# Optimization experiments

Measured on AMD Instinct MI355X. Metric: run time of the kernel, lower is better.

Reference implementation:

```python
import jax, jax.numpy as jnp
import numpy as np

N_EMBD = 1024
N_HEADS = 16
B, T = 4, 2048
EPS = 1e-5


def setup_inputs() -> dict:
    key = jax.random.key(0)
    ks = jax.random.split(key, 8)
    C = N_EMBD
    s = 0.02
    return {
        "x": jax.random.normal(ks[0], (B, T, C), dtype=jnp.float32),
        "ln1_w": jnp.ones((C,), jnp.float32),
        "ln1_b": jnp.zeros((C,), jnp.float32),
        "qkv_w": jax.random.normal(ks[1], (C, 3 * C), jnp.float32) * s,
        "qkv_b": jnp.zeros((3 * C,), jnp.float32),
        "proj_w": jax.random.normal(ks[2], (C, C), jnp.float32) * s,
        "proj_b": jnp.zeros((C,), jnp.float32),
        "ln2_w": jnp.ones((C,), jnp.float32),
        "ln2_b": jnp.zeros((C,), jnp.float32),
        "ff_w1": jax.random.normal(ks[3], (C, 4 * C), jnp.float32) * s,
        "ff_b1": jnp.zeros((4 * C,), jnp.float32),
        "ff_w2": jax.random.normal(ks[4], (4 * C, C), jnp.float32) * s,
        "ff_b2": jnp.zeros((C,), jnp.float32),
    }


def _layernorm(x, w, b):
    mu = jnp.mean(x, axis=-1, keepdims=True)
    var = jnp.mean(jnp.square(x - mu), axis=-1, keepdims=True)
    return (x - mu) * jax.lax.rsqrt(var + EPS) * w + b


def _block(x, ln1_w, ln1_b, qkv_w, qkv_b, proj_w, proj_b,
           ln2_w, ln2_b, ff_w1, ff_b1, ff_w2, ff_b2):
    Bb, Tt, C = x.shape
    hd = C // N_HEADS
    h = _layernorm(x, ln1_w, ln1_b)
    qkv = h @ qkv_w + qkv_b  # [B,T,3C]
    q, k, v = jnp.split(qkv, 3, axis=-1)
    q = q.reshape(Bb, Tt, N_HEADS, hd)
    k = k.reshape(Bb, Tt, N_HEADS, hd)
    v = v.reshape(Bb, Tt, N_HEADS, hd)
    # NOTE: original scales by 1/sqrt(C) (full embed dim), not 1/sqrt(head_dim)
    att = jnp.einsum("bqhd,bkhd->bhqk", q, k) * (1.0 / C ** 0.5)
    causal = jnp.tril(jnp.ones((Tt, Tt), dtype=bool))
    att = jnp.where(causal[None, None], att, -jnp.inf)
    att = jax.nn.softmax(att, axis=-1)
    y = jnp.einsum("bhqk,bkhd->bqhd", att, v).reshape(Bb, Tt, C)
    x = x + y @ proj_w + proj_b
    h2 = _layernorm(x, ln2_w, ln2_b)
    ff = jax.nn.relu(h2 @ ff_w1 + ff_b1) @ ff_w2 + ff_b2
    return x + ff


def reference(x, ln1_w, ln1_b, qkv_w, qkv_b, proj_w, proj_b,
              ln2_w, ln2_b, ff_w1, ff_b1, ff_w2, ff_b2):
    return _block(x, ln1_w, ln1_b, qkv_w, qkv_b, proj_w, proj_b,
                  ln2_w, ln2_b, ff_w1, ff_b1, ff_w2, ff_b2)
```

## Files before the change

### kernel.cpp

```cpp
#include <hip/hip_runtime.h>


typedef __attribute__((ext_vector_type(8))) short shortx8;
typedef __attribute__((ext_vector_type(4))) float floatx4;

__device__ __forceinline__ short f2bf(float f) {
  unsigned u = __builtin_bit_cast(unsigned, f);
  u = (u + 0x7fffu + ((u >> 16) & 1u)) >> 16;
  return (short)u;
}

__global__ __launch_bounds__(256)
void transpose_cast(const float* __restrict__ in, short* __restrict__ out,
                    int K, int N) {
  __shared__ float tile[32][33];
  const int n0 = blockIdx.x * 32, k0 = blockIdx.y * 32;
  const int tx = threadIdx.x & 31, ty = threadIdx.x >> 5;
  for (int i = 0; i < 32; i += 8)
    tile[ty + i][tx] = in[(size_t)(k0 + ty + i) * N + n0 + tx];
  __syncthreads();
  for (int i = 0; i < 32; i += 8)
    out[(size_t)(n0 + ty + i) * K + k0 + tx] = f2bf(tile[tx][ty + i]);
}

__global__ __launch_bounds__(256)
void layernorm_kernel(const float* __restrict__ x, const float* __restrict__ w,
                      const float* __restrict__ bta, short* __restrict__ out) {
  const int C = 1024;
  const int row = blockIdx.x;
  const float4 v = ((const float4*)(x + (size_t)row * C))[threadIdx.x];
  float s1 = v.x + v.y + v.z + v.w;
  float s2 = v.x * v.x + v.y * v.y + v.z * v.z + v.w * v.w;
  for (int m = 1; m < 64; m <<= 1) { s1 += __shfl_xor(s1, m); s2 += __shfl_xor(s2, m); }
  __shared__ float r1[4], r2[4];
  const int wid = threadIdx.x >> 6, lane = threadIdx.x & 63;
  if (lane == 0) { r1[wid] = s1; r2[wid] = s2; }
  __syncthreads();
  s1 = r1[0] + r1[1] + r1[2] + r1[3];
  s2 = r2[0] + r2[1] + r2[2] + r2[3];
  const float mean = s1 * (1.0f / C);
  const float var = s2 * (1.0f / C) - mean * mean;
  const float rs = rsqrtf(var + 1e-5f);
  const float4 wv = ((const float4*)w)[threadIdx.x];
  const float4 bv = ((const float4*)bta)[threadIdx.x];
  short4 o;
  o.x = f2bf((v.x - mean) * rs * wv.x + bv.x);
  o.y = f2bf((v.y - mean) * rs * wv.y + bv.y);
  o.z = f2bf((v.z - mean) * rs * wv.z + bv.z);
  o.w = f2bf((v.w - mean) * rs * wv.w + bv.w);
  *(short4*)(out + (size_t)row * C + threadIdx.x * 4) = o;
}

template<int FLAGS, typename OutT>
__global__ __launch_bounds__(256, 4)
void gemm_bt(const short* __restrict__ A, int lda,
             const short* __restrict__ Bt, int ldb,
             const float* __restrict__ bias, const float* __restrict__ resid,
             OutT* __restrict__ C, int M, int N, int K) {
  constexpr bool RELU = (FLAGS & 1) != 0;
  constexpr bool RESID = (FLAGS & 2) != 0;
  __shared__ short As[2][128 * 32];
  __shared__ short Bs[2][128 * 32];
  int bmi, bni;
  {
    const int nb = gridDim.x, mb = gridDim.y;
    const int g = blockIdx.x + nb * blockIdx.y;
    if ((mb & 7) == 0) {
      const int xcd = g & 7, l = g >> 3;
      bmi = xcd * (mb >> 3) + l / nb;
      bni = l % nb;
    } else { bmi = blockIdx.y; bni = blockIdx.x; }
  }
  const int bm0 = bmi * 128, bn0 = bni * 128;
  const int tid = threadIdx.x, wid = tid >> 6, lane = tid & 63;
  const int quad = lane >> 4, l15 = lane & 15;
  const int wm = wid & 1, wn = wid >> 1;
  const int srow = lane >> 2, scol = (lane & 3) * 8;
  floatx4 acc[4][4] = {};
  for (int k0 = 0; k0 < K; k0 += 64) {
    for (int i = 0; i < 2; ++i) {
      const int r0 = (wid * 2 + i) * 16;
      const short* ga = A + (size_t)(bm0 + r0 + srow) * lda + k0 + scol;
      const short* gb = Bt + (size_t)(bn0 + r0 + srow) * ldb + k0 + scol;
      __builtin_amdgcn_global_load_lds(
          (const __attribute__((address_space(1))) void*)ga,
          (__attribute__((address_space(3))) void*)&As[0][r0 * 32], 16, 0, 0);
      __builtin_amdgcn_global_load_lds(
          (const __attribute__((address_space(1))) void*)(ga + 32),
          (__attribute__((address_space(3))) void*)&As[1][r0 * 32], 16, 0, 0);
      __builtin_amdgcn_global_load_lds(
          (const __attribute__((address_space(1))) void*)gb,
          (__attribute__((address_space(3))) void*)&Bs[0][r0 * 32], 16, 0, 0);
      __builtin_amdgcn_global_load_lds(
          (const __attribute__((address_space(1))) void*)(gb + 32),
          (__attribute__((address_space(3))) void*)&Bs[1][r0 * 32], 16, 0, 0);
    }
    asm volatile("s_waitcnt vmcnt(0)" ::: "memory");
    __syncthreads();
    {
      shortx8 af[4], bfr[4];
#pragma unroll
      for (int i = 0; i < 4; ++i)
        af[i] = *(const shortx8*)&As[0][(wm * 64 + i * 16 + l15) * 32 + quad * 8];
#pragma unroll
      for (int j = 0; j < 4; ++j)
        bfr[j] = *(const shortx8*)&Bs[0][(wn * 64 + j * 16 + l15) * 32 + quad * 8];
#pragma unroll
      for (int i = 0; i < 4; ++i)
#pragma unroll
        for (int j = 0; j < 4; ++j)
          acc[i][j] = __builtin_amdgcn_mfma_f32_16x16x32_bf16(af[i], bfr[j], acc[i][j], 0, 0, 0);
    }
    {
      shortx8 af[4], bfr[4];
#pragma unroll
      for (int i = 0; i < 4; ++i)
        af[i] = *(const shortx8*)&As[1][(wm * 64 + i * 16 + l15) * 32 + quad * 8];
#pragma unroll
      for (int j = 0; j < 4; ++j)
        bfr[j] = *(const shortx8*)&Bs[1][(wn * 64 + j * 16 + l15) * 32 + quad * 8];
#pragma unroll
      for (int i = 0; i < 4; ++i)
#pragma unroll
        for (int j = 0; j < 4; ++j)
          acc[i][j] = __builtin_amdgcn_mfma_f32_16x16x32_bf16(af[i], bfr[j], acc[i][j], 0, 0, 0);
    }
    __syncthreads();
  }
#pragma unroll
  for (int i = 0; i < 4; ++i) {
    const int row = bm0 + wm * 64 + i * 16 + quad * 4;
#pragma unroll
    for (int j = 0; j < 4; ++j) {
      const int col = bn0 + wn * 64 + j * 16 + l15;
      const float bb = bias[col];
#pragma unroll
      for (int r = 0; r < 4; ++r) {
        float v = acc[i][j][r] + bb;
        if (RELU) v = fmaxf(v, 0.0f);
        if (RESID) v += resid[(size_t)(row + r) * N + col];
        if constexpr (sizeof(OutT) == 2)
          C[(size_t)(row + r) * N + col] = f2bf(v);
        else
          C[(size_t)(row + r) * N + col] = v;
      }
    }
  }
}

#define ATTN_SLOTS 80
#define ATTN_SLOT_F 4160

__global__ __launch_bounds__(256)
void attention_chunk(const short* __restrict__ qkv, short* __restrict__ y,
                     float* __restrict__ part) {
  constexpr int T = 2048, C = 1024, HD = 64, S3 = 3072;
  __shared__ short Ks[64 * 72];
  __shared__ short Vt[64 * 72];
  __shared__ short Ps[4][16 * 72];
  const int x = blockIdx.x, h = blockIdx.y, b = blockIdx.z;
  int qb, ch;
  if (x < 8)       { qb = x;                 ch = 0; }
  else if (x < 24) { qb = 8 + ((x - 8) >> 1);  ch = (x - 8) & 1; }
  else if (x < 48) { qb = 16 + (x - 24) / 3;   ch = (x - 24) % 3; }
  else             { qb = 24 + ((x - 48) >> 2); ch = (x - 48) & 3; }
  const int kt0 = ch * 8;
  const int kt1 = min(kt0 + 8, qb + 1);
  const int tid = threadIdx.x, wid = tid >> 6, lane = tid & 63;
  const int quad = lane >> 4, l15 = lane & 15;
  const size_t base = (size_t)b * T * S3;
  const int q0 = qb * 64 + wid * 16;
  const short* Qp = qkv + base + (size_t)(q0 + l15) * S3 + h * HD;
  const shortx8 qf0 = *(const shortx8*)(Qp + quad * 8);
  const shortx8 qf1 = *(const shortx8*)(Qp + 32 + quad * 8);
  floatx4 o[4] = {};
  float lsum[4] = {0.f, 0.f, 0.f, 0.f};
  const float scale2 = 0.03125f * 1.44269504088896f;
  const int skey = tid >> 2, sd = (tid & 3) * 16;
  const int vkp = tid & 31, vdb = tid >> 5;
  const int vkE = (vkp >> 4) * 32 + (vkp & 15);
  const short* Kbase = qkv + base + C + h * HD;
  const short* Vbase = qkv + base + 2 * C + h * HD;
  shortx8 pk0, pk1, pv0, pv1;
  {
    const short* Kp = Kbase + (size_t)(kt0 * 64 + skey) * S3 + sd;
    pk0 = *(const shortx8*)Kp;
    pk1 = *(const shortx8*)(Kp + 8);
    const short* Vp = Vbase + (size_t)(kt0 * 64 + vkE) * S3 + vdb * 8;
    pv0 = *(const shortx8*)Vp;
    pv1 = *(const shortx8*)(Vp + 16 * S3);
  }
  for (int kt = kt0; kt < kt1; ++kt) {
    const int key0 = kt * 64;
    __syncthreads();
    *(shortx8*)&Ks[skey * 72 + sd] = pk0;
    *(shortx8*)&Ks[skey * 72 + sd + 8] = pk1;
#pragma unroll
    for (int j = 0; j < 8; ++j) {
      short2 pr = make_short2(pv0[j], pv1[j]);
      *(short2*)&Vt[(vdb * 8 + j) * 72 + 2 * vkp] = pr;
    }
    __syncthreads();
    if (kt + 1 < kt1) {
      const int kn = key0 + 64;
      const short* Kp = Kbase + (size_t)(kn + skey) * S3 + sd;
      pk0 = *(const shortx8*)Kp;
      pk1 = *(const shortx8*)(Kp + 8);
      const short* Vp = Vbase + (size_t)(kn + vkE) * S3 + vdb * 8;
      pv0 = *(const shortx8*)Vp;
      pv1 = *(const shortx8*)(Vp + 16 * S3);
    }
    floatx4 s[4];
#pragma unroll
    for (int nt = 0; nt < 4; ++nt) {
      const short* kb = &Ks[(nt * 16 + l15) * 72 + quad * 8];
      floatx4 a = {};
      a = __builtin_amdgcn_mfma_f32_16x16x32_bf16(qf0, *(const shortx8*)kb, a, 0, 0, 0);
      a = __builtin_amdgcn_mfma_f32_16x16x32_bf16(qf1, *(const shortx8*)(kb + 32), a, 0, 0, 0);
      s[nt] = a;
    }
    short* pw = &Ps[wid][0];
    const bool diag = (kt == qb);
#pragma unroll
    for (int r = 0; r < 4; ++r) {
      float pr[4];
#pragma unroll
      for (int nt = 0; nt < 4; ++nt) {
        float sv = s[nt][r] * scale2;
        if (diag) {
          const int key = key0 + nt * 16 + l15;
          const int q = q0 + quad * 4 + r;
          if (key > q) sv = -INFINITY;
        }
        const float p = exp2f(sv);
        lsum[r] += p;
        pr[nt] = p;
      }
      unsigned w0, w1;
      asm("v_cvt_pk_bf16_f32 %0, %1, %2" : "=v"(w0) : "v"(pr[0]), "v"(pr[1]));
      asm("v_cvt_pk_bf16_f32 %0, %1, %2" : "=v"(w1) : "v"(pr[2]), "v"(pr[3]));
      unsigned* prow = (unsigned*)&pw[(quad * 4 + r) * 72];
      prow[l15] = w0;
      prow[16 + l15] = w1;
    }
    asm volatile("s_waitcnt lgkmcnt(0)" ::: "memory");
#pragma unroll
    for (int kf = 0; kf < 2; ++kf) {
      const shortx8 pa = *(const shortx8*)&Ps[wid][l15 * 72 + kf * 32 + quad * 8];
#pragma unroll
      for (int dt = 0; dt < 4; ++dt) {
        const shortx8 vb = *(const shortx8*)&Vt[(dt * 16 + l15) * 72 + kf * 32 + quad * 8];
        o[dt] = __builtin_amdgcn_mfma_f32_16x16x32_bf16(pa, vb, o[dt], 0, 0, 0);
      }
    }
  }
  float ls[4];
#pragma unroll
  for (int r = 0; r < 4; ++r) {
    float s = lsum[r];
    for (int off = 1; off < 16; off <<= 1) s += __shfl_xor(s, off);
    ls[r] = s;
  }
  if (x < 8) {
#pragma unroll
    for (int dt = 0; dt < 4; ++dt)
#pragma unroll
      for (int r = 0; r < 4; ++r) {
        const int q = q0 + quad * 4 + r;
        y[((size_t)b * T + q) * C + h * HD + dt * 16 + l15] =
            f2bf(o[dt][r] / ls[r]);
      }
  } else {
    float* pp = part + ((size_t)(b * 16 + h) * ATTN_SLOTS + x) * ATTN_SLOT_F;
    const int qw = wid * 16;
#pragma unroll
    for (int dt = 0; dt < 4; ++dt)
#pragma unroll
      for (int r = 0; r < 4; ++r)
        pp[(qw + quad * 4 + r) * 64 + dt * 16 + l15] = o[dt][r];
    if (l15 == 0)
#pragma unroll
      for (int r = 0; r < 4; ++r)
        pp[4096 + qw + quad * 4 + r] = ls[r];
  }
}

__global__ __launch_bounds__(256)
void attn_reduce(const float* __restrict__ part, short* __restrict__ y) {
  constexpr int T = 2048, C = 1024;
  const int qb = 8 + blockIdx.x, h = blockIdx.y, b = blockIdx.z;
  const int c = qb / 8 + 1;
  int slot0;
  if (qb < 16)      slot0 = 8 + 2 * (qb - 8);
  else if (qb < 24) slot0 = 24 + 3 * (qb - 16);
  else              slot0 = 48 + 4 * (qb - 24);
  const float* rb = part + ((size_t)(b * 16 + h) * ATTN_SLOTS + slot0) * ATTN_SLOT_F;
  const int t = threadIdx.x;
  const int q = t >> 2, dg = (t & 3) * 16;
  float acc[16] = {};
  float ls = 0.f;
  for (int ci = 0; ci < c; ++ci) {
    const float* pp = rb + (size_t)ci * ATTN_SLOT_F;
    const float4* op = (const float4*)(pp + q * 64 + dg);
#pragma unroll
    for (int i = 0; i < 4; ++i) {
      float4 v = op[i];
      acc[4 * i + 0] += v.x; acc[4 * i + 1] += v.y;
      acc[4 * i + 2] += v.z; acc[4 * i + 3] += v.w;
    }
    ls += pp[4096 + q];
  }
  const float inv = 1.0f / ls;
  short o16[16];
#pragma unroll
  for (int i = 0; i < 16; ++i) o16[i] = f2bf(acc[i] * inv);
  short* yp = y + ((size_t)b * T + qb * 64 + q) * C + h * 64 + dg;
  *(shortx8*)yp = *(shortx8*)&o16[0];
  *(shortx8*)(yp + 8) = *(shortx8*)&o16[8];
}

__global__ __launch_bounds__(256)
void attention_kernel(const short* __restrict__ qkv, short* __restrict__ y) {
  constexpr int T = 2048, C = 1024, HD = 64, S3 = 3072;
  __shared__ short Ks[64 * 72];
  __shared__ short Vt[64 * 72];
  __shared__ short Ps[4][16 * 72];
  const int qb = blockIdx.x, h = blockIdx.y, b = blockIdx.z;
  const int tid = threadIdx.x, wid = tid >> 6, lane = tid & 63;
  const int quad = lane >> 4, l15 = lane & 15;
  const size_t base = (size_t)b * T * S3;
  const int q0 = qb * 64 + wid * 16;
  const short* Qp = qkv + base + (size_t)(q0 + l15) * S3 + h * HD;
  const shortx8 qf0 = *(const shortx8*)(Qp + quad * 8);
  const shortx8 qf1 = *(const shortx8*)(Qp + 32 + quad * 8);
  floatx4 o[4] = {};
  float lsum[4] = {0.f, 0.f, 0.f, 0.f};
  const float scale2 = 0.03125f * 1.44269504088896f;
  const int skey = tid >> 2, sd = (tid & 3) * 16;
  const int vkp = tid & 31, vdb = tid >> 5;
  for (int kt = 0; kt <= qb; ++kt) {
    const int key0 = kt * 64;
    __syncthreads();
    {
      const short* Kp = qkv + base + (size_t)(key0 + skey) * S3 + C + h * HD + sd;
      shortx8 ka = *(const shortx8*)Kp;
      shortx8 kb = *(const shortx8*)(Kp + 8);
      *(shortx8*)&Ks[skey * 72 + sd] = ka;
      *(shortx8*)&Ks[skey * 72 + sd + 8] = kb;
      const short* Vp = qkv + base + (size_t)(key0 + 2 * vkp) * S3 + 2 * C + h * HD + vdb * 8;
      shortx8 va = *(const shortx8*)Vp;
      shortx8 vb = *(const shortx8*)(Vp + S3);
#pragma unroll
      for (int j = 0; j < 8; ++j) {
        short2 pr = make_short2(va[j], vb[j]);
        *(short2*)&Vt[(vdb * 8 + j) * 72 + 2 * vkp] = pr;
      }
    }
    __syncthreads();
    floatx4 s[4];
#pragma unroll
    for (int nt = 0; nt < 4; ++nt) {
      const short* kb = &Ks[(nt * 16 + l15) * 72 + quad * 8];
      floatx4 a = {};
      a = __builtin_amdgcn_mfma_f32_16x16x32_bf16(qf0, *(const shortx8*)kb, a, 0, 0, 0);
      a = __builtin_amdgcn_mfma_f32_16x16x32_bf16(qf1, *(const shortx8*)(kb + 32), a, 0, 0, 0);
      s[nt] = a;
    }
    short* pw = &Ps[wid][0];
    const bool diag = (kt == qb);
#pragma unroll
    for (int nt = 0; nt < 4; ++nt)
#pragma unroll
      for (int r = 0; r < 4; ++r) {
        float sv = s[nt][r] * scale2;
        if (diag) {
          const int key = key0 + nt * 16 + l15;
          const int q = q0 + quad * 4 + r;
          if (key > q) sv = -INFINITY;
        }
        const float p = exp2f(sv);
        lsum[r] += p;
        pw[(quad * 4 + r) * 72 + nt * 16 + l15] = f2bf(p);
      }
    asm volatile("s_waitcnt lgkmcnt(0)" ::: "memory");
#pragma unroll
    for (int kf = 0; kf < 2; ++kf) {
      const shortx8 pa = *(const shortx8*)&Ps[wid][l15 * 72 + kf * 32 + quad * 8];
#pragma unroll
      for (int dt = 0; dt < 4; ++dt) {
        const shortx8 vb = *(const shortx8*)&Vt[(dt * 16 + l15) * 72 + kf * 32 + quad * 8];
        o[dt] = __builtin_amdgcn_mfma_f32_16x16x32_bf16(pa, vb, o[dt], 0, 0, 0);
      }
    }
  }
  float inv[4];
#pragma unroll
  for (int r = 0; r < 4; ++r) {
    float s = lsum[r];
    for (int off = 1; off < 16; off <<= 1) s += __shfl_xor(s, off);
    inv[r] = 1.0f / s;
  }
#pragma unroll
  for (int dt = 0; dt < 4; ++dt)
#pragma unroll
    for (int r = 0; r < 4; ++r) {
      const int q = q0 + quad * 4 + r;
      y[((size_t)b * T + q) * C + h * HD + dt * 16 + l15] = f2bf(o[dt][r] * inv[r]);
    }
}

extern "C" void kernel_launch(void* const* d_in, const int* in_sizes, int n_in,
                              void* d_out, int out_size, void* d_ws, size_t ws_size,
                              hipStream_t stream) {
  const float* x      = (const float*)d_in[0];
  const float* ln1_w  = (const float*)d_in[1];
  const float* ln1_b  = (const float*)d_in[2];
  const float* qkv_w  = (const float*)d_in[3];
  const float* qkv_b  = (const float*)d_in[4];
  const float* proj_w = (const float*)d_in[5];
  const float* proj_b = (const float*)d_in[6];
  const float* ln2_w  = (const float*)d_in[7];
  const float* ln2_b  = (const float*)d_in[8];
  const float* ff_w1  = (const float*)d_in[9];
  const float* ff_b1  = (const float*)d_in[10];
  const float* ff_w2  = (const float*)d_in[11];
  const float* ff_b2  = (const float*)d_in[12];
  float* out = (float*)d_out;

  char* p = (char*)d_ws;
  short* wT_qkv  = (short*)p; p += (size_t)3072 * 1024 * 2;
  short* wT_proj = (short*)p; p += (size_t)1024 * 1024 * 2;
  short* wT_ff1  = (short*)p; p += (size_t)4096 * 1024 * 2;
  short* wT_ff2  = (short*)p; p += (size_t)1024 * 4096 * 2;
  short* act16   = (short*)p; p += (size_t)8192 * 1024 * 2;
  short* big     = (short*)p; p += (size_t)8192 * 4096 * 2;
  float* part    = (float*)p;
  const size_t need = (size_t)(p - (char*)d_ws) +
                      (size_t)64 * ATTN_SLOTS * ATTN_SLOT_F * 4;
  const bool split = (ws_size >= need);

  transpose_cast<<<dim3(96, 32), 256, 0, stream>>>(qkv_w, wT_qkv, 1024, 3072);
  transpose_cast<<<dim3(32, 32), 256, 0, stream>>>(proj_w, wT_proj, 1024, 1024);
  transpose_cast<<<dim3(128, 32), 256, 0, stream>>>(ff_w1, wT_ff1, 1024, 4096);
  transpose_cast<<<dim3(32, 128), 256, 0, stream>>>(ff_w2, wT_ff2, 4096, 1024);

  layernorm_kernel<<<8192, 256, 0, stream>>>(x, ln1_w, ln1_b, act16);
  gemm_bt<0, short><<<dim3(24, 64), 256, 0, stream>>>(
      act16, 1024, wT_qkv, 1024, qkv_b, nullptr, big, 8192, 3072, 1024);
  if (split) {
    attention_chunk<<<dim3(ATTN_SLOTS, 16, 4), 256, 0, stream>>>(big, act16, part);
    attn_reduce<<<dim3(24, 16, 4), 256, 0, stream>>>(part, act16);
  } else {
    attention_kernel<<<dim3(32, 16, 4), 256, 0, stream>>>(big, act16);
  }
  gemm_bt<2, float><<<dim3(8, 64), 256, 0, stream>>>(
      act16, 1024, wT_proj, 1024, proj_b, x, out, 8192, 1024, 1024);
  layernorm_kernel<<<8192, 256, 0, stream>>>(out, ln2_w, ln2_b, act16);
  gemm_bt<1, short><<<dim3(32, 64), 256, 0, stream>>>(
      act16, 1024, wT_ff1, 1024, ff_b1, nullptr, big, 8192, 4096, 1024);
  gemm_bt<2, float><<<dim3(8, 64), 256, 0, stream>>>(
      big, 4096, wT_ff2, 4096, ff_b2, out, out, 8192, 1024, 4096);
}
```

Measured before the change: 498.1 us.

## Process two query blocks per attention chunk to reuse staged K/V tiles

Each attention_chunk workgroup now covers 128 queries (two 64-row sub-blocks) instead of 64, so every K/V tile loaded into shared memory feeds twice the MFMA work. The grid shrinks from 80 to 40 slots per head, the partial-slot size doubles, and attn_reduce is rewritten to combine 128-row slots with 32 columns per thread. This is meant to halve global K/V traffic and staging overhead. In exchange it doubles the accumulator registers, with launch bounds set to allow 4 blocks, and reduces the number of workgroups, which may lower occupancy and worsen load balance.

```diff
diff --git a/kernel.cpp b/kernel.cpp
--- a/kernel.cpp
+++ b/kernel.cpp
@@ -148,10 +148,10 @@
   }
 }
 
-#define ATTN_SLOTS 80
-#define ATTN_SLOT_F 4160
-
-__global__ __launch_bounds__(256)
+#define ATTN_SLOTS 40
+#define ATTN_SLOT_F 8320
+
+__global__ __launch_bounds__(256, 4)
 void attention_chunk(const short* __restrict__ qkv, short* __restrict__ y,
                      float* __restrict__ part) {
   constexpr int T = 2048, C = 1024, HD = 64, S3 = 3072;
@@ -159,22 +159,26 @@
   __shared__ short Vt[64 * 72];
   __shared__ short Ps[4][16 * 72];
   const int x = blockIdx.x, h = blockIdx.y, b = blockIdx.z;
-  int qb, ch;
-  if (x < 8)       { qb = x;                 ch = 0; }
-  else if (x < 24) { qb = 8 + ((x - 8) >> 1);  ch = (x - 8) & 1; }
-  else if (x < 48) { qb = 16 + (x - 24) / 3;   ch = (x - 24) % 3; }
-  else             { qb = 24 + ((x - 48) >> 2); ch = (x - 48) & 3; }
+  int qb0, ch;
+  if (x < 4)       { qb0 = x;                    ch = 0; }
+  else if (x < 12) { qb0 = 4 + ((x - 4) >> 1);   ch = (x - 4) & 1; }
+  else if (x < 24) { qb0 = 8 + (x - 12) / 3;     ch = (x - 12) % 3; }
+  else             { qb0 = 12 + ((x - 24) >> 2); ch = (x - 24) & 3; }
   const int kt0 = ch * 8;
-  const int kt1 = min(kt0 + 8, qb + 1);
+  const int kt1 = min(kt0 + 8, 2 * qb0 + 2);
   const int tid = threadIdx.x, wid = tid >> 6, lane = tid & 63;
   const int quad = lane >> 4, l15 = lane & 15;
   const size_t base = (size_t)b * T * S3;
-  const int q0 = qb * 64 + wid * 16;
-  const short* Qp = qkv + base + (size_t)(q0 + l15) * S3 + h * HD;
-  const shortx8 qf0 = *(const shortx8*)(Qp + quad * 8);
-  const shortx8 qf1 = *(const shortx8*)(Qp + 32 + quad * 8);
-  floatx4 o[4] = {};
-  float lsum[4] = {0.f, 0.f, 0.f, 0.f};
+  const int Q0 = qb0 * 128;
+  shortx8 qf[2][2];
+#pragma unroll
+  for (int s = 0; s < 2; ++s) {
+    const short* Qp = qkv + base + (size_t)(Q0 + s * 64 + wid * 16 + l15) * S3 + h * HD;
+    qf[s][0] = *(const shortx8*)(Qp + quad * 8);
+    qf[s][1] = *(const shortx8*)(Qp + 32 + quad * 8);
+  }
+  floatx4 o[2][4] = {};
+  float lsum[2][4] = {};
   const float scale2 = 0.03125f * 1.44269504088896f;
   const int skey = tid >> 2, sd = (tid & 3) * 16;
   const int vkp = tid & 31, vdb = tid >> 5;
@@ -210,113 +214,127 @@
       pv0 = *(const shortx8*)Vp;
       pv1 = *(const shortx8*)(Vp + 16 * S3);
     }
-    floatx4 s[4];
-#pragma unroll
-    for (int nt = 0; nt < 4; ++nt) {
-      const short* kb = &Ks[(nt * 16 + l15) * 72 + quad * 8];
-      floatx4 a = {};
-      a = __builtin_amdgcn_mfma_f32_16x16x32_bf16(qf0, *(const shortx8*)kb, a, 0, 0, 0);
-      a = __builtin_amdgcn_mfma_f32_16x16x32_bf16(qf1, *(const shortx8*)(kb + 32), a, 0, 0, 0);
-      s[nt] = a;
-    }
-    short* pw = &Ps[wid][0];
-    const bool diag = (kt == qb);
+#pragma unroll
+    for (int s = 0; s < 2; ++s) {
+      const int lim = 2 * qb0 + s;
+      if (kt > lim) continue;
+      const int q0s = Q0 + s * 64 + wid * 16;
+      floatx4 sc[4];
+#pragma unroll
+      for (int nt = 0; nt < 4; ++nt) {
+        const short* kb = &Ks[(nt * 16 + l15) * 72 + quad * 8];
+        floatx4 a = {};
+        a = __builtin_amdgcn_mfma_f32_16x16x32_bf16(qf[s][0], *(const shortx8*)kb, a, 0, 0, 0);
+        a = __builtin_amdgcn_mfma_f32_16x16x32_bf16(qf[s][1], *(const shortx8*)(kb + 32), a, 0, 0, 0);
+        sc[nt] = a;
+      }
+      short* pw = &Ps[wid][0];
+      const bool diag = (kt == lim);
+#pragma unroll
+      for (int r = 0; r < 4; ++r) {
+        float pr[4];
+#pragma unroll
+        for (int nt = 0; nt < 4; ++nt) {
+          float sv = sc[nt][r] * scale2;
+          if (diag) {
+            const int key = key0 + nt * 16 + l15;
+            const int q = q0s + quad * 4 + r;
+            if (key > q) sv = -INFINITY;
+          }
+          const float p = exp2f(sv);
+          lsum[s][r] += p;
+          pr[nt] = p;
+        }
+        unsigned w0, w1;
+        asm("v_cvt_pk_bf16_f32 %0, %1, %2" : "=v"(w0) : "v"(pr[0]), "v"(pr[1]));
+        asm("v_cvt_pk_bf16_f32 %0, %1, %2" : "=v"(w1) : "v"(pr[2]), "v"(pr[3]));
+        unsigned* prow = (unsigned*)&pw[(quad * 4 + r) * 72];
+        prow[l15] = w0;
+        prow[16 + l15] = w1;
+      }
+      asm volatile("s_waitcnt lgkmcnt(0)" ::: "memory");
+#pragma unroll
+      for (int kf = 0; kf < 2; ++kf) {
+        const shortx8 pa = *(const shortx8*)&Ps[wid][l15 * 72 + kf * 32 + quad * 8];
+#pragma unroll
+        for (int dt = 0; dt < 4; ++dt) {
+          const shortx8 vb = *(const shortx8*)&Vt[(dt * 16 + l15) * 72 + kf * 32 + quad * 8];
+          o[s][dt] = __builtin_amdgcn_mfma_f32_16x16x32_bf16(pa, vb, o[s][dt], 0, 0, 0);
+        }
+      }
+    }
+  }
+  float ls[2][4];
+#pragma unroll
+  for (int s = 0; s < 2; ++s)
 #pragma unroll
     for (int r = 0; r < 4; ++r) {
-      float pr[4];
-#pragma unroll
-      for (int nt = 0; nt < 4; ++nt) {
-        float sv = s[nt][r] * scale2;
-        if (diag) {
-          const int key = key0 + nt * 16 + l15;
-          const int q = q0 + quad * 4 + r;
-          if (key > q) sv = -INFINITY;
+      float v = lsum[s][r];
+      for (int off = 1; off < 16; off <<= 1) v += __shfl_xor(v, off);
+      ls[s][r] = v;
+    }
+  if (x < 4) {
+#pragma unroll
+    for (int s = 0; s < 2; ++s)
+#pragma unroll
+      for (int dt = 0; dt < 4; ++dt)
+#pragma unroll
+        for (int r = 0; r < 4; ++r) {
+          const int q = Q0 + s * 64 + wid * 16 + quad * 4 + r;
+          y[((size_t)b * T + q) * C + h * HD + dt * 16 + l15] =
+              f2bf(o[s][dt][r] / ls[s][r]);
         }
-        const float p = exp2f(sv);
-        lsum[r] += p;
-        pr[nt] = p;
-      }
-      unsigned w0, w1;
-      asm("v_cvt_pk_bf16_f32 %0, %1, %2" : "=v"(w0) : "v"(pr[0]), "v"(pr[1]));
-      asm("v_cvt_pk_bf16_f32 %0, %1, %2" : "=v"(w1) : "v"(pr[2]), "v"(pr[3]));
-      unsigned* prow = (unsigned*)&pw[(quad * 4 + r) * 72];
-      prow[l15] = w0;
-      prow[16 + l15] = w1;
-    }
-    asm volatile("s_waitcnt lgkmcnt(0)" ::: "memory");
-#pragma unroll
-    for (int kf = 0; kf < 2; ++kf) {
-      const shortx8 pa = *(const shortx8*)&Ps[wid][l15 * 72 + kf * 32 + quad * 8];
-#pragma unroll
-      for (int dt = 0; dt < 4; ++dt) {
-        const shortx8 vb = *(const shortx8*)&Vt[(dt * 16 + l15) * 72 + kf * 32 + quad * 8];
-        o[dt] = __builtin_amdgcn_mfma_f32_16x16x32_bf16(pa, vb, o[dt], 0, 0, 0);
-      }
-    }
-  }
-  float ls[4];
-#pragma unroll
-  for (int r = 0; r < 4; ++r) {
-    float s = lsum[r];
-    for (int off = 1; off < 16; off <<= 1) s += __shfl_xor(s, off);
-    ls[r] = s;
-  }
-  if (x < 8) {
-#pragma unroll
-    for (int dt = 0; dt < 4; ++dt)
-#pragma unroll
-      for (int r = 0; r < 4; ++r) {
-        const int q = q0 + quad * 4 + r;
-        y[((size_t)b * T + q) * C + h * HD + dt * 16 + l15] =
-            f2bf(o[dt][r] / ls[r]);
-      }
   } else {
     float* pp = part + ((size_t)(b * 16 + h) * ATTN_SLOTS + x) * ATTN_SLOT_F;
-    const int qw = wid * 16;
-#pragma unroll
-    for (int dt = 0; dt < 4; ++dt)
-#pragma unroll
-      for (int r = 0; r < 4; ++r)
-        pp[(qw + quad * 4 + r) * 64 + dt * 16 + l15] = o[dt][r];
-    if (l15 == 0)
-#pragma unroll
-      for (int r = 0; r < 4; ++r)
-        pp[4096 + qw + quad * 4 + r] = ls[r];
+#pragma unroll
+    for (int s = 0; s < 2; ++s) {
+      const int rw = s * 64 + wid * 16;
+#pragma unroll
+      for (int dt = 0; dt < 4; ++dt)
+#pragma unroll
+        for (int r = 0; r < 4; ++r)
+          pp[(rw + quad * 4 + r) * 64 + dt * 16 + l15] = o[s][dt][r];
+      if (l15 == 0)
+#pragma unroll
+        for (int r = 0; r < 4; ++r)
+          pp[8192 + rw + quad * 4 + r] = ls[s][r];
+    }
   }
 }
 
 __global__ __launch_bounds__(256)
 void attn_reduce(const float* __restrict__ part, short* __restrict__ y) {
   constexpr int T = 2048, C = 1024;
-  const int qb = 8 + blockIdx.x, h = blockIdx.y, b = blockIdx.z;
-  const int c = qb / 8 + 1;
+  const int qb0 = 4 + blockIdx.x, h = blockIdx.y, b = blockIdx.z;
+  const int c = qb0 / 4 + 1;
   int slot0;
-  if (qb < 16)      slot0 = 8 + 2 * (qb - 8);
-  else if (qb < 24) slot0 = 24 + 3 * (qb - 16);
-  else              slot0 = 48 + 4 * (qb - 24);
+  if (qb0 < 8)       slot0 = 4 + 2 * (qb0 - 4);
+  else if (qb0 < 12) slot0 = 12 + 3 * (qb0 - 8);
+  else               slot0 = 24 + 4 * (qb0 - 12);
   const float* rb = part + ((size_t)(b * 16 + h) * ATTN_SLOTS + slot0) * ATTN_SLOT_F;
   const int t = threadIdx.x;
-  const int q = t >> 2, dg = (t & 3) * 16;
-  float acc[16] = {};
+  const int q = t >> 1, dg = (t & 1) * 32;
+  float acc[32] = {};
   float ls = 0.f;
   for (int ci = 0; ci < c; ++ci) {
     const float* pp = rb + (size_t)ci * ATTN_SLOT_F;
     const float4* op = (const float4*)(pp + q * 64 + dg);
 #pragma unroll
-    for (int i = 0; i < 4; ++i) {
+    for (int i = 0; i < 8; ++i) {
       float4 v = op[i];
       acc[4 * i + 0] += v.x; acc[4 * i + 1] += v.y;
       acc[4 * i + 2] += v.z; acc[4 * i + 3] += v.w;
     }
-    ls += pp[4096 + q];
+    ls += pp[8192 + q];
   }
   const float inv = 1.0f / ls;
-  short o16[16];
-#pragma unroll
-  for (int i = 0; i < 16; ++i) o16[i] = f2bf(acc[i] * inv);
-  short* yp = y + ((size_t)b * T + qb * 64 + q) * C + h * 64 + dg;
-  *(shortx8*)yp = *(shortx8*)&o16[0];
-  *(shortx8*)(yp + 8) = *(shortx8*)&o16[8];
+  short o16[32];
+#pragma unroll
+  for (int i = 0; i < 32; ++i) o16[i] = f2bf(acc[i] * inv);
+  short* yp = y + ((size_t)b * T + qb0 * 128 + q) * C + h * 64 + dg;
+#pragma unroll
+  for (int i = 0; i < 4; ++i)
+    *(shortx8*)(yp + 8 * i) = *(shortx8*)&o16[8 * i];
 }
 
 __global__ __launch_bounds__(256)
@@ -449,7 +467,7 @@
       act16, 1024, wT_qkv, 1024, qkv_b, nullptr, big, 8192, 3072, 1024);
   if (split) {
     attention_chunk<<<dim3(ATTN_SLOTS, 16, 4), 256, 0, stream>>>(big, act16, part);
-    attn_reduce<<<dim3(24, 16, 4), 256, 0, stream>>>(part, act16);
+    attn_reduce<<<dim3(12, 16, 4), 256, 0, stream>>>(part, act16);
   } else {
     attention_kernel<<<dim3(32, 16, 4), 256, 0, stream>>>(big, act16);
   }
```

Measured after the change: 536.3 us. +7.7%, slower.
